# Kernel tuning notes

Hardware: AMD Instinct MI355X
Metric: run time of the kernel (lower is better)

## Reference

```python
import jax, jax.numpy as jnp
import numpy as np

IN_F, OUT_F, RANK = 4096, 4096, 64
B, S = 4, 2048


def setup_inputs() -> dict:
    key = jax.random.key(0)
    k1, k2, k3 = jax.random.split(key, 3)
    x = jax.random.normal(k1, (B, S, IN_F), dtype=jnp.float32)
    # Low-rank compressed weight factors: W = U @ V^T, shape [OUT_F, IN_F]
    U = jax.random.normal(k2, (OUT_F, RANK), dtype=jnp.float32) / np.sqrt(RANK)
    V = jax.random.normal(k3, (IN_F, RANK), dtype=jnp.float32) / np.sqrt(IN_F)
    bias = jnp.zeros((OUT_F,), dtype=jnp.float32)
    return {"x": x, "U": U, "V": V, "bias": bias}


def reference(x, U, V, bias):
    # Decompress: weight = compressor.decompress(compressed_weight) -> [out, in]
    weight = jnp.einsum("or,ir->oi", U, V)  # materialized like the original
    # F.linear(x, weight, bias) = x @ weight^T + bias
    return jnp.einsum("bsi,oi->bso", x, weight) + bias
```

## Files before the change

kernel.cpp:

```cpp
#include <hip/hip_runtime.h>

#define IN_F    4096
#define OUT_F   4096
#define RANK    64
#define M_TOTAL 8192
#define M_TILE  16
#define BLOCK   512
#define NWAVES  8

using short8  = __attribute__((ext_vector_type(8))) short;
using float4v = __attribute__((ext_vector_type(4))) float;

#define MFMA16(A, B, C) __builtin_amdgcn_mfma_f32_16x16x32_bf16((A), (B), (C), 0, 0, 0)

__device__ __forceinline__ void split2(float x, short& h, short& l) {
    unsigned u = __float_as_uint(x);
    unsigned t = u & 0xffff0000u;
    h = (short)(t >> 16);
    float r = x - __uint_as_float(t);
    l = (short)(__float_as_uint(r) >> 16);
}

__device__ __forceinline__ void split_f4x2(float4 a, float4 b, short8& hi, short8& lo) {
    short h0,h1,h2,h3,h4,h5,h6,h7, l0,l1,l2,l3,l4,l5,l6,l7;
    split2(a.x,h0,l0); split2(a.y,h1,l1); split2(a.z,h2,l2); split2(a.w,h3,l3);
    split2(b.x,h4,l4); split2(b.y,h5,l5); split2(b.z,h6,l6); split2(b.w,h7,l7);
    hi = (short8){h0,h1,h2,h3,h4,h5,h6,h7};
    lo = (short8){l0,l1,l2,l3,l4,l5,l6,l7};
}


__global__ void prep_uv(const float* __restrict__ V, const float* __restrict__ U,
                        unsigned short* __restrict__ vt_hi, unsigned short* __restrict__ vt_lo,
                        unsigned short* __restrict__ u_hi,  unsigned short* __restrict__ u_lo)
{
    const int b = blockIdx.x;
    const int linear = (b & 255) * 256 + threadIdx.x;
    short h[4], l[4];
    if (b < 256) {
        const int r  = linear >> 10;
        const int k0 = (linear & 1023) * 4;
        #pragma unroll
        for (int i = 0; i < 4; ++i)
            split2(V[(size_t)(k0 + i) * RANK + r], h[i], l[i]);
        const size_t o = (size_t)r * IN_F + k0;
        *(ushort4*)(vt_hi + o) = make_ushort4((unsigned short)h[0], (unsigned short)h[1],
                                              (unsigned short)h[2], (unsigned short)h[3]);
        *(ushort4*)(vt_lo + o) = make_ushort4((unsigned short)l[0], (unsigned short)l[1],
                                              (unsigned short)l[2], (unsigned short)l[3]);
    } else {
        const int idx = linear * 4;
        const float4 u4 = *(const float4*)(U + idx);
        split2(u4.x, h[0], l[0]); split2(u4.y, h[1], l[1]);
        split2(u4.z, h[2], l[2]); split2(u4.w, h[3], l[3]);
        *(ushort4*)(u_hi + idx) = make_ushort4((unsigned short)h[0], (unsigned short)h[1],
                                               (unsigned short)h[2], (unsigned short)h[3]);
        *(ushort4*)(u_lo + idx) = make_ushort4((unsigned short)l[0], (unsigned short)l[1],
                                               (unsigned short)l[2], (unsigned short)l[3]);
    }
}

__global__ __launch_bounds__(BLOCK, 4) void lowrank_xv(
    const float* __restrict__ x,
    const unsigned short* __restrict__ vt_hi, const unsigned short* __restrict__ vt_lo,
    unsigned short* __restrict__ t_hi, unsigned short* __restrict__ t_lo)
{
    __shared__ float part[NWAVES][M_TILE][RANK + 4];

    const int tid  = threadIdx.x;
    const int wv   = tid >> 6;
    const int lane = tid & 63;
    const int l15  = lane & 15;
    const int quad = lane >> 4;
    const int m0   = blockIdx.x * M_TILE;

    float4v acc[4] = {};
    const float*          xp = x     + (size_t)(m0 + l15) * IN_F + wv * 512 + quad * 8;
    const unsigned short* vh = vt_hi + (size_t)l15 * IN_F + wv * 512 + quad * 8;
    const unsigned short* vl = vt_lo + (size_t)l15 * IN_F + wv * 512 + quad * 8;

    float4 xa = *(const float4*)(xp);
    float4 xb = *(const float4*)(xp + 4);
    #pragma unroll
    for (int ks = 0; ks < 16; ++ks) {
        const int k0 = ks * 32;
        float4 na = xa, nb = xb;
        if (ks < 15) {
            na = *(const float4*)(xp + k0 + 32);
            nb = *(const float4*)(xp + k0 + 36);
        }
        short8 a_hi, a_lo;
        split_f4x2(xa, xb, a_hi, a_lo);
        #pragma unroll
        for (int rt = 0; rt < 4; ++rt) {
            short8 b_hi = *(const short8*)(vh + (size_t)rt * 16 * IN_F + k0);
            short8 b_lo = *(const short8*)(vl + (size_t)rt * 16 * IN_F + k0);
            acc[rt] = MFMA16(a_lo, b_hi, acc[rt]);
            acc[rt] = MFMA16(a_hi, b_lo, acc[rt]);
            acc[rt] = MFMA16(a_hi, b_hi, acc[rt]);
        }
        xa = na; xb = nb;
    }

    #pragma unroll
    for (int rt = 0; rt < 4; ++rt)
        #pragma unroll
        for (int rg = 0; rg < 4; ++rg)
            part[wv][quad * 4 + rg][rt * 16 + l15] = acc[rt][rg];
    __syncthreads();

    const int e = tid * 2;
    const int m = e >> 6, r = e & 63;
    float s0 = 0.f, s1 = 0.f;
    #pragma unroll
    for (int w = 0; w < NWAVES; ++w) { s0 += part[w][m][r]; s1 += part[w][m][r + 1]; }
    short h0, l0, h1, l1;
    split2(s0, h0, l0); split2(s1, h1, l1);
    const size_t off = (size_t)m0 * RANK + e;
    *(ushort2*)(t_hi + off) = make_ushort2((unsigned short)h0, (unsigned short)h1);
    *(ushort2*)(t_lo + off) = make_ushort2((unsigned short)l0, (unsigned short)l1);
}

__global__ __launch_bounds__(256, 4) void lowrank_tu(
    const unsigned short* __restrict__ t_hi, const unsigned short* __restrict__ t_lo,
    const unsigned short* __restrict__ u_hi, const unsigned short* __restrict__ u_lo,
    const float* __restrict__ bias, float* __restrict__ out)
{
    const int tid  = threadIdx.x;
    const int wv   = tid >> 6;
    const int lane = tid & 63;
    const int l15  = lane & 15;
    const int quad = lane >> 4;
    const int og   = blockIdx.x & 7;
    const int mg   = blockIdx.x >> 3;
    const int m0   = mg * 64 + wv * 16;
    const int o0   = og * 512;

    short8 ta_hi[2], ta_lo[2];
    {
        const unsigned short* tp_h = t_hi + (size_t)(m0 + l15) * RANK + quad * 8;
        const unsigned short* tp_l = t_lo + (size_t)(m0 + l15) * RANK + quad * 8;
        ta_hi[0] = *(const short8*)(tp_h);   ta_hi[1] = *(const short8*)(tp_h + 32);
        ta_lo[0] = *(const short8*)(tp_l);   ta_lo[1] = *(const short8*)(tp_l + 32);
    }

    #pragma unroll 2
    for (int nt = 0; nt < 32; ++nt) {
        const int o = o0 + nt * 16 + l15;
        const unsigned short* up_h = u_hi + (size_t)o * RANK + quad * 8;
        const unsigned short* up_l = u_lo + (size_t)o * RANK + quad * 8;
        const float bv = bias[o];
        float4v acc = {bv, bv, bv, bv};
        #pragma unroll
        for (int ks = 0; ks < 2; ++ks) {
            short8 uh = *(const short8*)(up_h + ks * 32);
            short8 ul = *(const short8*)(up_l + ks * 32);
            acc = MFMA16(ta_lo[ks], uh, acc);
            acc = MFMA16(ta_hi[ks], ul, acc);
            acc = MFMA16(ta_hi[ks], uh, acc);
        }
        float* op = out + (size_t)(m0 + quad * 4) * OUT_F + o;
        op[0 * OUT_F] = acc[0];
        op[1 * OUT_F] = acc[1];
        op[2 * OUT_F] = acc[2];
        op[3 * OUT_F] = acc[3];
    }
}


__global__ void prep_v(const float* __restrict__ V, unsigned short* __restrict__ vt_hi,
                       unsigned short* __restrict__ vt_lo) {
    int linear = blockIdx.x * 256 + threadIdx.x;
    int r  = linear >> 10;
    int k0 = (linear & 1023) * 4;
    short h[4], l[4];
    #pragma unroll
    for (int i = 0; i < 4; ++i)
        split2(V[(size_t)(k0 + i) * RANK + r], h[i], l[i]);
    size_t o = (size_t)r * IN_F + k0;
    *(ushort4*)(vt_hi + o) = make_ushort4((unsigned short)h[0], (unsigned short)h[1],
                                          (unsigned short)h[2], (unsigned short)h[3]);
    *(ushort4*)(vt_lo + o) = make_ushort4((unsigned short)l[0], (unsigned short)l[1],
                                          (unsigned short)l[2], (unsigned short)l[3]);
}

__global__ __launch_bounds__(BLOCK, 4) void fused_lowrank_mfma(
    const float* __restrict__ x, const float* __restrict__ U,
    const float* __restrict__ bias, const unsigned short* __restrict__ vt_hi,
    const unsigned short* __restrict__ vt_lo, float* __restrict__ out)
{
    __shared__ float part[NWAVES][M_TILE][RANK + 4];
    __shared__ unsigned short t_hi[M_TILE][RANK + 8];
    __shared__ unsigned short t_lo[M_TILE][RANK + 8];

    const int tid  = threadIdx.x;
    const int wv   = tid >> 6;
    const int lane = tid & 63;
    const int l15  = lane & 15;
    const int quad = lane >> 4;
    const int m0   = blockIdx.x * M_TILE;

    float4v acc[4] = {};
    const float*          xp = x     + (size_t)(m0 + l15) * IN_F + quad * 8;
    const unsigned short* vh = vt_hi + (size_t)l15 * IN_F + quad * 8;
    const unsigned short* vl = vt_lo + (size_t)l15 * IN_F + quad * 8;

    #pragma unroll 2
    for (int ks = 0; ks < 16; ++ks) {
        const int k0 = wv * 512 + ks * 32;
        float4 xa = *(const float4*)(xp + k0);
        float4 xb = *(const float4*)(xp + k0 + 4);
        short8 a_hi, a_lo;
        split_f4x2(xa, xb, a_hi, a_lo);
        #pragma unroll
        for (int rt = 0; rt < 4; ++rt) {
            short8 b_hi = *(const short8*)(vh + (size_t)rt * 16 * IN_F + k0);
            short8 b_lo = *(const short8*)(vl + (size_t)rt * 16 * IN_F + k0);
            acc[rt] = MFMA16(a_lo, b_hi, acc[rt]);
            acc[rt] = MFMA16(a_hi, b_lo, acc[rt]);
            acc[rt] = MFMA16(a_hi, b_hi, acc[rt]);
        }
    }

    #pragma unroll
    for (int rt = 0; rt < 4; ++rt)
        #pragma unroll
        for (int rg = 0; rg < 4; ++rg)
            part[wv][quad * 4 + rg][rt * 16 + l15] = acc[rt][rg];
    __syncthreads();

    {
        const int e = tid * 2;
        const int m = e >> 6, r = e & 63;
        float s0 = 0.f, s1 = 0.f;
        #pragma unroll
        for (int w = 0; w < NWAVES; ++w) { s0 += part[w][m][r]; s1 += part[w][m][r + 1]; }
        short h0, l0, h1, l1;
        split2(s0, h0, l0); split2(s1, h1, l1);
        t_hi[m][r]     = (unsigned short)h0;  t_lo[m][r]     = (unsigned short)l0;
        t_hi[m][r + 1] = (unsigned short)h1;  t_lo[m][r + 1] = (unsigned short)l1;
    }
    __syncthreads();

    short8 ta_hi[2], ta_lo[2];
    #pragma unroll
    for (int ks = 0; ks < 2; ++ks) {
        ta_hi[ks] = *(const short8*)(&t_hi[l15][ks * 32 + quad * 8]);
        ta_lo[ks] = *(const short8*)(&t_lo[l15][ks * 32 + quad * 8]);
    }

    for (int nt = 0; nt < 32; ++nt) {
        const int o0 = wv * 512 + nt * 16;
        const int o  = o0 + l15;
        const float* Up = U + (size_t)o * RANK + quad * 8;
        const float bv = bias[o];
        float4v acc2 = {bv, bv, bv, bv};
        #pragma unroll
        for (int ks = 0; ks < 2; ++ks) {
            float4 u0 = *(const float4*)(Up + ks * 32);
            float4 u1 = *(const float4*)(Up + ks * 32 + 4);
            short8 u_hi, u_lo;
            split_f4x2(u0, u1, u_hi, u_lo);
            acc2 = MFMA16(ta_lo[ks], u_hi, acc2);
            acc2 = MFMA16(ta_hi[ks], u_lo, acc2);
            acc2 = MFMA16(ta_hi[ks], u_hi, acc2);
        }
        float* op = out + (size_t)(m0 + quad * 4) * OUT_F + o;
        op[0 * OUT_F] = acc2[0];
        op[1 * OUT_F] = acc2[1];
        op[2 * OUT_F] = acc2[2];
        op[3 * OUT_F] = acc2[3];
    }
}

__global__ __launch_bounds__(256, 2) void fallback_fp32(
    const float* __restrict__ x, const float* __restrict__ U,
    const float* __restrict__ V, const float* __restrict__ bias,
    float* __restrict__ out)
{
    __shared__ float v_lds[128][RANK];
    __shared__ float t_lds[8][RANK];
    const int tid = threadIdx.x, lane = tid & 63, wave = tid >> 6;
    const int m0 = blockIdx.x * 8;
    float acc0 = 0.f, acc1 = 0.f;
    const size_t row_base = (size_t)(m0 + wave * 2) * IN_F;
    for (int kt = 0; kt < IN_F; kt += 128) {
        const float4* Vg = (const float4*)(V + (size_t)kt * RANK);
        float4* Vs = (float4*)(&v_lds[0][0]);
        #pragma unroll
        for (int i = 0; i < 8; ++i) Vs[tid + 256 * i] = Vg[tid + 256 * i];
        __syncthreads();
        const float* xp = x + row_base + kt;
        #pragma unroll 8
        for (int k = 0; k < 128; k += 4) {
            float v0 = v_lds[k+0][lane], v1 = v_lds[k+1][lane];
            float v2 = v_lds[k+2][lane], v3 = v_lds[k+3][lane];
            float4 xa = *(const float4*)(xp + 0 * IN_F + k);
            float4 xb = *(const float4*)(xp + 1 * IN_F + k);
            acc0 += xa.x*v0 + xa.y*v1 + xa.z*v2 + xa.w*v3;
            acc1 += xb.x*v0 + xb.y*v1 + xb.z*v2 + xb.w*v3;
        }
        __syncthreads();
    }
    t_lds[wave*2+0][lane] = acc0;
    t_lds[wave*2+1][lane] = acc1;
    __syncthreads();
    for (int oc = 0; oc < OUT_F; oc += 1024) {
        const int o4 = oc + tid * 4;
        const float4 b4 = *(const float4*)(bias + o4);
        float4 a0=b4,a1=b4,a2=b4,a3=b4,a4=b4,a5=b4,a6=b4,a7=b4;
        const float* Up = U + (size_t)o4 * RANK;
        #pragma unroll 2
        for (int r0 = 0; r0 < RANK; r0 += 4) {
            const float4 u0 = *(const float4*)(Up + 0*RANK + r0);
            const float4 u1 = *(const float4*)(Up + 1*RANK + r0);
            const float4 u2 = *(const float4*)(Up + 2*RANK + r0);
            const float4 u3 = *(const float4*)(Up + 3*RANK + r0);
            #define P2_STEP(AM, MM) { \
                const float4 t4 = *(const float4*)(&t_lds[MM][r0]); \
                AM.x += t4.x*u0.x + t4.y*u0.y + t4.z*u0.z + t4.w*u0.w; \
                AM.y += t4.x*u1.x + t4.y*u1.y + t4.z*u1.z + t4.w*u1.w; \
                AM.z += t4.x*u2.x + t4.y*u2.y + t4.z*u2.z + t4.w*u2.w; \
                AM.w += t4.x*u3.x + t4.y*u3.y + t4.z*u3.z + t4.w*u3.w; }
            P2_STEP(a0,0) P2_STEP(a1,1) P2_STEP(a2,2) P2_STEP(a3,3)
            P2_STEP(a4,4) P2_STEP(a5,5) P2_STEP(a6,6) P2_STEP(a7,7)
            #undef P2_STEP
        }
        float* op = out + (size_t)m0 * OUT_F + o4;
        *(float4*)(op+0*OUT_F)=a0; *(float4*)(op+1*OUT_F)=a1;
        *(float4*)(op+2*OUT_F)=a2; *(float4*)(op+3*OUT_F)=a3;
        *(float4*)(op+4*OUT_F)=a4; *(float4*)(op+5*OUT_F)=a5;
        *(float4*)(op+6*OUT_F)=a6; *(float4*)(op+7*OUT_F)=a7;
    }
}

extern "C" void kernel_launch(void* const* d_in, const int* in_sizes, int n_in,
                              void* d_out, int out_size, void* d_ws, size_t ws_size,
                              hipStream_t stream) {
    const float* x    = (const float*)d_in[0];
    const float* U    = (const float*)d_in[1];
    const float* V    = (const float*)d_in[2];
    const float* bias = (const float*)d_in[3];
    float* out = (float*)d_out;

    const size_t E = (size_t)RANK * IN_F;
    const size_t T = (size_t)M_TOTAL * RANK;
    const size_t need_full  = (E * 4 + T * 2) * sizeof(unsigned short);
    const size_t need_fused = (E * 2) * sizeof(unsigned short);

    if (ws_size >= need_full) {
        unsigned short* vt_hi = (unsigned short*)d_ws;
        unsigned short* vt_lo = vt_hi + E;
        unsigned short* u_hi  = vt_lo + E;
        unsigned short* u_lo  = u_hi  + E;
        unsigned short* t_hi  = u_lo  + E;
        unsigned short* t_lo  = t_hi  + T;
        prep_uv<<<dim3(512), dim3(256), 0, stream>>>(V, U, vt_hi, vt_lo, u_hi, u_lo);
        lowrank_xv<<<dim3(M_TOTAL / M_TILE), dim3(BLOCK), 0, stream>>>(
            x, vt_hi, vt_lo, t_hi, t_lo);
        lowrank_tu<<<dim3((M_TOTAL / 64) * (OUT_F / 512)), dim3(256), 0, stream>>>(
            t_hi, t_lo, u_hi, u_lo, bias, out);
    } else if (ws_size >= need_fused) {
        unsigned short* vt_hi = (unsigned short*)d_ws;
        unsigned short* vt_lo = vt_hi + E;
        prep_v<<<dim3(256), dim3(256), 0, stream>>>(V, vt_hi, vt_lo);
        fused_lowrank_mfma<<<dim3(M_TOTAL / M_TILE), dim3(BLOCK), 0, stream>>>(
            x, U, bias, vt_hi, vt_lo, out);
    } else {
        fallback_fp32<<<dim3(M_TOTAL / 8), dim3(256), 0, stream>>>(x, U, V, bias, out);
    }
}
```

Measured before the change: 327.3 us.

## Split-K the x·V stage across blocks with separate reduction kernel

Adds a new path that splits the K dimension of x·V across four blocks per 32-row group, writes fp32 partial sums to workspace, reduces and splits them to bf16 hi/lo in a separate kernel, then runs a retiled T·U kernel with prefetched U fragments. The goal is more parallelism and occupancy in the bandwidth-heavy x read, plus software prefetching of x and U loads. The cost is an extra kernel launch and extra workspace traffic for the partial sums, and the path only runs if the workspace is large enough. The older fused single-kernel fallback is removed.

Result: slower. 379.2 us (+15.8%).

```diff
diff --git a/kernel.cpp b/kernel.cpp
--- a/kernel.cpp
+++ b/kernel.cpp
@@ -7,6 +7,8 @@
 #define M_TILE  16
 #define BLOCK   512
 #define NWAVES  8
+#define KSPLIT  4
+#define XV_MT   32
 
 using short8  = __attribute__((ext_vector_type(8))) short;
 using float4v = __attribute__((ext_vector_type(4))) float;
@@ -60,6 +62,149 @@
     }
 }
 
+__global__ __launch_bounds__(512, 8) void lowrank_xv2(
+    const float* __restrict__ x,
+    const unsigned short* __restrict__ vt_hi, const unsigned short* __restrict__ vt_lo,
+    float* __restrict__ t_part)
+{
+    __shared__ float part[KSPLIT][XV_MT][RANK + 4];
+
+    const int tid  = threadIdx.x;
+    const int wv   = tid >> 6;
+    const int msub = wv >> 2;
+    const int ksub = wv & 3;
+    const int lane = tid & 63;
+    const int l15  = lane & 15;
+    const int quad = lane >> 4;
+    const int kq   = blockIdx.x & 3;
+    const int mg   = blockIdx.x >> 2;
+    const int m0   = mg * XV_MT;
+    const int kbase = kq * 1024 + ksub * 256;
+
+    float4v acc[4] = {};
+    const float*          xp = x     + (size_t)(m0 + msub * 16 + l15) * IN_F + kbase + quad * 8;
+    const unsigned short* vh = vt_hi + (size_t)l15 * IN_F + kbase + quad * 8;
+    const unsigned short* vl = vt_lo + (size_t)l15 * IN_F + kbase + quad * 8;
+
+    float4 xa = *(const float4*)(xp);
+    float4 xb = *(const float4*)(xp + 4);
+    #pragma unroll
+    for (int ks = 0; ks < 8; ++ks) {
+        const int k0 = ks * 32;
+        float4 na = xa, nb = xb;
+        if (ks < 7) {
+            na = *(const float4*)(xp + k0 + 32);
+            nb = *(const float4*)(xp + k0 + 36);
+        }
+        short8 a_hi, a_lo;
+        split_f4x2(xa, xb, a_hi, a_lo);
+        #pragma unroll
+        for (int rt = 0; rt < 4; ++rt) {
+            short8 b_hi = *(const short8*)(vh + (size_t)rt * 16 * IN_F + k0);
+            short8 b_lo = *(const short8*)(vl + (size_t)rt * 16 * IN_F + k0);
+            acc[rt] = MFMA16(a_lo, b_hi, acc[rt]);
+            acc[rt] = MFMA16(a_hi, b_lo, acc[rt]);
+            acc[rt] = MFMA16(a_hi, b_hi, acc[rt]);
+        }
+        xa = na; xb = nb;
+    }
+
+    #pragma unroll
+    for (int rt = 0; rt < 4; ++rt)
+        #pragma unroll
+        for (int rg = 0; rg < 4; ++rg)
+            part[ksub][msub * 16 + quad * 4 + rg][rt * 16 + l15] = acc[rt][rg];
+    __syncthreads();
+
+    const int e = tid * 4;
+    const int m = e >> 6, r = e & 63;
+    float4 s = {0.f, 0.f, 0.f, 0.f};
+    #pragma unroll
+    for (int ks2 = 0; ks2 < KSPLIT; ++ks2) {
+        const float4 p4 = *(const float4*)(&part[ks2][m][r]);
+        s.x += p4.x; s.y += p4.y; s.z += p4.z; s.w += p4.w;
+    }
+    *(float4*)(t_part + (size_t)kq * (M_TOTAL * RANK) + (size_t)(m0 + m) * RANK + r) = s;
+}
+
+__global__ void reduce_t(const float* __restrict__ t_part,
+                         unsigned short* __restrict__ t_hi, unsigned short* __restrict__ t_lo)
+{
+    const size_t e = (size_t)(blockIdx.x * 256 + threadIdx.x) * 4;
+    float4 s = *(const float4*)(t_part + e);
+    #pragma unroll
+    for (int p = 1; p < KSPLIT; ++p) {
+        const float4 a = *(const float4*)(t_part + (size_t)p * (M_TOTAL * RANK) + e);
+        s.x += a.x; s.y += a.y; s.z += a.z; s.w += a.w;
+    }
+    short h[4], l[4];
+    split2(s.x, h[0], l[0]); split2(s.y, h[1], l[1]);
+    split2(s.z, h[2], l[2]); split2(s.w, h[3], l[3]);
+    *(ushort4*)(t_hi + e) = make_ushort4((unsigned short)h[0], (unsigned short)h[1],
+                                         (unsigned short)h[2], (unsigned short)h[3]);
+    *(ushort4*)(t_lo + e) = make_ushort4((unsigned short)l[0], (unsigned short)l[1],
+                                         (unsigned short)l[2], (unsigned short)l[3]);
+}
+
+__global__ __launch_bounds__(256, 8) void lowrank_tu2(
+    const unsigned short* __restrict__ t_hi, const unsigned short* __restrict__ t_lo,
+    const unsigned short* __restrict__ u_hi, const unsigned short* __restrict__ u_lo,
+    const float* __restrict__ bias, float* __restrict__ out)
+{
+    const int tid  = threadIdx.x;
+    const int wv   = tid >> 6;
+    const int lane = tid & 63;
+    const int l15  = lane & 15;
+    const int quad = lane >> 4;
+    const int og   = blockIdx.x & 15;
+    const int mg   = blockIdx.x >> 4;
+    const int m0   = mg * 64 + wv * 16;
+    const int o0   = og * 256;
+
+    short8 ta_hi[2], ta_lo[2];
+    {
+        const unsigned short* tp_h = t_hi + (size_t)(m0 + l15) * RANK + quad * 8;
+        const unsigned short* tp_l = t_lo + (size_t)(m0 + l15) * RANK + quad * 8;
+        ta_hi[0] = *(const short8*)(tp_h);   ta_hi[1] = *(const short8*)(tp_h + 32);
+        ta_lo[0] = *(const short8*)(tp_l);   ta_lo[1] = *(const short8*)(tp_l + 32);
+    }
+
+    const unsigned short* up_h = u_hi + (size_t)(o0 + l15) * RANK + quad * 8;
+    const unsigned short* up_l = u_lo + (size_t)(o0 + l15) * RANK + quad * 8;
+    short8 uh0 = *(const short8*)(up_h);
+    short8 uh1 = *(const short8*)(up_h + 32);
+    short8 ul0 = *(const short8*)(up_l);
+    short8 ul1 = *(const short8*)(up_l + 32);
+
+    #pragma unroll 2
+    for (int nt = 0; nt < 16; ++nt) {
+        short8 nh0 = uh0, nh1 = uh1, nl0 = ul0, nl1 = ul1;
+        if (nt < 15) {
+            const int adv = (nt + 1) * 16 * RANK;
+            nh0 = *(const short8*)(up_h + adv);
+            nh1 = *(const short8*)(up_h + adv + 32);
+            nl0 = *(const short8*)(up_l + adv);
+            nl1 = *(const short8*)(up_l + adv + 32);
+        }
+        const int o = o0 + nt * 16 + l15;
+        const float bv = bias[o];
+        float4v acc = {bv, bv, bv, bv};
+        acc = MFMA16(ta_lo[0], uh0, acc);
+        acc = MFMA16(ta_hi[0], ul0, acc);
+        acc = MFMA16(ta_hi[0], uh0, acc);
+        acc = MFMA16(ta_lo[1], uh1, acc);
+        acc = MFMA16(ta_hi[1], ul1, acc);
+        acc = MFMA16(ta_hi[1], uh1, acc);
+        float* op = out + (size_t)(m0 + quad * 4) * OUT_F + o;
+        op[0 * OUT_F] = acc[0];
+        op[1 * OUT_F] = acc[1];
+        op[2 * OUT_F] = acc[2];
+        op[3 * OUT_F] = acc[3];
+        uh0 = nh0; uh1 = nh1; ul0 = nl0; ul1 = nl1;
+    }
+}
+
+
 __global__ __launch_bounds__(BLOCK, 4) void lowrank_xv(
     const float* __restrict__ x,
     const unsigned short* __restrict__ vt_hi, const unsigned short* __restrict__ vt_lo,
@@ -164,112 +309,6 @@
         op[1 * OUT_F] = acc[1];
         op[2 * OUT_F] = acc[2];
         op[3 * OUT_F] = acc[3];
-    }
-}
-
-
-__global__ void prep_v(const float* __restrict__ V, unsigned short* __restrict__ vt_hi,
-                       unsigned short* __restrict__ vt_lo) {
-    int linear = blockIdx.x * 256 + threadIdx.x;
-    int r  = linear >> 10;
-    int k0 = (linear & 1023) * 4;
-    short h[4], l[4];
-    #pragma unroll
-    for (int i = 0; i < 4; ++i)
-        split2(V[(size_t)(k0 + i) * RANK + r], h[i], l[i]);
-    size_t o = (size_t)r * IN_F + k0;
-    *(ushort4*)(vt_hi + o) = make_ushort4((unsigned short)h[0], (unsigned short)h[1],
-                                          (unsigned short)h[2], (unsigned short)h[3]);
-    *(ushort4*)(vt_lo + o) = make_ushort4((unsigned short)l[0], (unsigned short)l[1],
-                                          (unsigned short)l[2], (unsigned short)l[3]);
-}
-
-__global__ __launch_bounds__(BLOCK, 4) void fused_lowrank_mfma(
-    const float* __restrict__ x, const float* __restrict__ U,
-    const float* __restrict__ bias, const unsigned short* __restrict__ vt_hi,
-    const unsigned short* __restrict__ vt_lo, float* __restrict__ out)
-{
-    __shared__ float part[NWAVES][M_TILE][RANK + 4];
-    __shared__ unsigned short t_hi[M_TILE][RANK + 8];
-    __shared__ unsigned short t_lo[M_TILE][RANK + 8];
-
-    const int tid  = threadIdx.x;
-    const int wv   = tid >> 6;
-    const int lane = tid & 63;
-    const int l15  = lane & 15;
-    const int quad = lane >> 4;
-    const int m0   = blockIdx.x * M_TILE;
-
-    float4v acc[4] = {};
-    const float*          xp = x     + (size_t)(m0 + l15) * IN_F + quad * 8;
-    const unsigned short* vh = vt_hi + (size_t)l15 * IN_F + quad * 8;
-    const unsigned short* vl = vt_lo + (size_t)l15 * IN_F + quad * 8;
-
-    #pragma unroll 2
-    for (int ks = 0; ks < 16; ++ks) {
-        const int k0 = wv * 512 + ks * 32;
-        float4 xa = *(const float4*)(xp + k0);
-        float4 xb = *(const float4*)(xp + k0 + 4);
-        short8 a_hi, a_lo;
-        split_f4x2(xa, xb, a_hi, a_lo);
-        #pragma unroll
-        for (int rt = 0; rt < 4; ++rt) {
-            short8 b_hi = *(const short8*)(vh + (size_t)rt * 16 * IN_F + k0);
-            short8 b_lo = *(const short8*)(vl + (size_t)rt * 16 * IN_F + k0);
-            acc[rt] = MFMA16(a_lo, b_hi, acc[rt]);
-            acc[rt] = MFMA16(a_hi, b_lo, acc[rt]);
-            acc[rt] = MFMA16(a_hi, b_hi, acc[rt]);
-        }
-    }
-
-    #pragma unroll
-    for (int rt = 0; rt < 4; ++rt)
-        #pragma unroll
-        for (int rg = 0; rg < 4; ++rg)
-            part[wv][quad * 4 + rg][rt * 16 + l15] = acc[rt][rg];
-    __syncthreads();
-
-    {
-        const int e = tid * 2;
-        const int m = e >> 6, r = e & 63;
-        float s0 = 0.f, s1 = 0.f;
-        #pragma unroll
-        for (int w = 0; w < NWAVES; ++w) { s0 += part[w][m][r]; s1 += part[w][m][r + 1]; }
-        short h0, l0, h1, l1;
-        split2(s0, h0, l0); split2(s1, h1, l1);
-        t_hi[m][r]     = (unsigned short)h0;  t_lo[m][r]     = (unsigned short)l0;
-        t_hi[m][r + 1] = (unsigned short)h1;  t_lo[m][r + 1] = (unsigned short)l1;
-    }
-    __syncthreads();
-
-    short8 ta_hi[2], ta_lo[2];
-    #pragma unroll
-    for (int ks = 0; ks < 2; ++ks) {
-        ta_hi[ks] = *(const short8*)(&t_hi[l15][ks * 32 + quad * 8]);
-        ta_lo[ks] = *(const short8*)(&t_lo[l15][ks * 32 + quad * 8]);
-    }
-
-    for (int nt = 0; nt < 32; ++nt) {
-        const int o0 = wv * 512 + nt * 16;
-        const int o  = o0 + l15;
-        const float* Up = U + (size_t)o * RANK + quad * 8;
-        const float bv = bias[o];
-        float4v acc2 = {bv, bv, bv, bv};
-        #pragma unroll
-        for (int ks = 0; ks < 2; ++ks) {
-            float4 u0 = *(const float4*)(Up + ks * 32);
-            float4 u1 = *(const float4*)(Up + ks * 32 + 4);
-            short8 u_hi, u_lo;
-            split_f4x2(u0, u1, u_hi, u_lo);
-            acc2 = MFMA16(ta_lo[ks], u_hi, acc2);
-            acc2 = MFMA16(ta_hi[ks], u_lo, acc2);
-            acc2 = MFMA16(ta_hi[ks], u_hi, acc2);
-        }
-        float* op = out + (size_t)(m0 + quad * 4) * OUT_F + o;
-        op[0 * OUT_F] = acc2[0];
-        op[1 * OUT_F] = acc2[1];
-        op[2 * OUT_F] = acc2[2];
-        op[3 * OUT_F] = acc2[3];
     }
 }
 
@@ -345,10 +384,25 @@
 
     const size_t E = (size_t)RANK * IN_F;
     const size_t T = (size_t)M_TOTAL * RANK;
-    const size_t need_full  = (E * 4 + T * 2) * sizeof(unsigned short);
-    const size_t need_fused = (E * 2) * sizeof(unsigned short);
-
-    if (ws_size >= need_full) {
+    const size_t need_v3 = (E * 4 + T * 2) * sizeof(unsigned short)
+                         + (size_t)KSPLIT * T * sizeof(float);
+    const size_t need_v2 = (E * 4 + T * 2) * sizeof(unsigned short);
+
+    if (ws_size >= need_v3) {
+        unsigned short* vt_hi = (unsigned short*)d_ws;
+        unsigned short* vt_lo = vt_hi + E;
+        unsigned short* u_hi  = vt_lo + E;
+        unsigned short* u_lo  = u_hi  + E;
+        unsigned short* t_hi  = u_lo  + E;
+        unsigned short* t_lo  = t_hi  + T;
+        float*          t_part = (float*)(t_lo + T);
+        prep_uv<<<dim3(512), dim3(256), 0, stream>>>(V, U, vt_hi, vt_lo, u_hi, u_lo);
+        lowrank_xv2<<<dim3((M_TOTAL / XV_MT) * KSPLIT), dim3(512), 0, stream>>>(
+            x, vt_hi, vt_lo, t_part);
+        reduce_t<<<dim3(T / (256 * 4)), dim3(256), 0, stream>>>(t_part, t_hi, t_lo);
+        lowrank_tu2<<<dim3((M_TOTAL / 64) * (OUT_F / 256)), dim3(256), 0, stream>>>(
+            t_hi, t_lo, u_hi, u_lo, bias, out);
+    } else if (ws_size >= need_v2) {
         unsigned short* vt_hi = (unsigned short*)d_ws;
         unsigned short* vt_lo = vt_hi + E;
         unsigned short* u_hi  = vt_lo + E;
@@ -360,12 +414,6 @@
             x, vt_hi, vt_lo, t_hi, t_lo);
         lowrank_tu<<<dim3((M_TOTAL / 64) * (OUT_F / 512)), dim3(256), 0, stream>>>(
             t_hi, t_lo, u_hi, u_lo, bias, out);
-    } else if (ws_size >= need_fused) {
-        unsigned short* vt_hi = (unsigned short*)d_ws;
-        unsigned short* vt_lo = vt_hi + E;
-        prep_v<<<dim3(256), dim3(256), 0, stream>>>(V, vt_hi, vt_lo);
-        fused_lowrank_mfma<<<dim3(M_TOTAL / M_TILE), dim3(BLOCK), 0, stream>>>(
-            x, U, bias, vt_hi, vt_lo, out);
     } else {
         fallback_fp32<<<dim3(M_TOTAL / 8), dim3(256), 0, stream>>>(x, U, V, bias, out);
     }
```
